# Kernel tuning notes

Measured on AMD Instinct MI355X. Metric: run time of the kernel, lower is better.

Reference implementation:

```python
import jax, jax.numpy as jnp
import numpy as np
from jax import lax

EPS = 1e-3  # BatchNorm1d eps from norm_fn
SPARSE_SHAPE = (41, 200, 176)  # (z, y, x)
IN_CH = 4


def _conv3d(x, w, stride, pad):
    # x: [N,C,D,H,W], w: [O,I,kd,kh,kw]
    return lax.conv_general_dilated(x, w, window_strides=stride, padding=pad,
                                    dimension_numbers=('NCDHW', 'OIDHW', 'NCDHW'))


def _bn_relu(y, bn, mask):
    # eval-mode BatchNorm1d over active voxels == per-channel affine; inactive sites
    # must stay exactly 0 in a sparse tensor, hence the final mask multiply.
    g, b, m, v = bn[0], bn[1], bn[2], bn[3]
    scale = g * lax.rsqrt(v + EPS)
    shift = b - m * scale
    y = y * scale[None, :, None, None, None] + shift[None, :, None, None, None]
    return jax.nn.relu(y) * mask


def _subm(x, mask, w, bn):
    # SubMConv3d: conv evaluated only at existing active sites; active set unchanged.
    kd, kh, kw = w.shape[2:]
    pad = [(kd // 2, kd // 2), (kh // 2, kh // 2), (kw // 2, kw // 2)]
    return _bn_relu(_conv3d(x, w, (1, 1, 1), pad), bn, mask)


def _spconv(x, mask, w, bn, stride, pad):
    # SparseConv3d: output active set = sites with >=1 active input in receptive field.
    pads = [(p, p) for p in pad]
    y = _conv3d(x, w, stride, pads)
    k = tuple(w.shape[2:])
    new_mask = lax.reduce_window(mask, 0.0, lax.max, (1, 1) + k, (1, 1) + tuple(stride),
                                 [(0, 0), (0, 0)] + pads)
    new_mask = (new_mask > 0).astype(x.dtype)
    return _bn_relu(y, bn, new_mask), new_mask


def setup_inputs() -> dict:
    key = jax.random.key(0)
    ks = jax.random.split(key, 16)
    D, H, W = SPARSE_SHAPE
    mask = (jax.random.uniform(ks[0], (1, 1, D, H, W)) < 0.02).astype(jnp.float32)
    x = jax.random.normal(ks[1], (1, IN_CH, D, H, W), jnp.float32) * mask
    specs = [(16, IN_CH, (3, 3, 3)), (16, 16, (3, 3, 3)),
             (32, 16, (3, 3, 3)), (32, 32, (3, 3, 3)), (32, 32, (3, 3, 3)),
             (64, 32, (3, 3, 3)), (64, 64, (3, 3, 3)), (64, 64, (3, 3, 3)),
             (64, 64, (3, 3, 3)), (64, 64, (3, 3, 3)), (64, 64, (3, 3, 3)),
             (128, 64, (3, 1, 1))]
    inp = {'x': x, 'mask': mask}
    for i, (co, ci, k) in enumerate(specs):
        kk = jax.random.fold_in(ks[2], i)
        fan = ci * k[0] * k[1] * k[2]
        inp['w%d' % i] = jax.random.normal(kk, (co, ci) + k, jnp.float32) / np.sqrt(fan).astype(np.float32)
        inp['bn%d' % i] = jnp.stack([
            jax.random.uniform(jax.random.fold_in(kk, 1), (co,), minval=0.5, maxval=1.5),
            jax.random.normal(jax.random.fold_in(kk, 2), (co,)) * 0.1,
            jax.random.normal(jax.random.fold_in(kk, 3), (co,)) * 0.1,
            jax.random.uniform(jax.random.fold_in(kk, 4), (co,), minval=0.5, maxval=1.5)])
    return inp


def reference(x, mask, w0, bn0, w1, bn1, w2, bn2, w3, bn3, w4, bn4, w5, bn5,
              w6, bn6, w7, bn7, w8, bn8, w9, bn9, w10, bn10, w11, bn11):
    h = _subm(x, mask, w0, bn0)                       # conv_input (subm1)
    h = _subm(h, mask, w1, bn1)                       # conv1 -> x_conv1
    h, m2 = _spconv(h, mask, w2, bn2, (2, 2, 2), (1, 1, 1))  # conv2 down
    h = _subm(h, m2, w3, bn3)
    h = _subm(h, m2, w4, bn4)                         # x_conv2
    h, m3 = _spconv(h, m2, w5, bn5, (2, 2, 2), (1, 1, 1))    # conv3 down
    h = _subm(h, m3, w6, bn6)
    h = _subm(h, m3, w7, bn7)                         # x_conv3
    h, m4 = _spconv(h, m3, w8, bn8, (2, 2, 2), (0, 1, 1))    # conv4 down
    h = _subm(h, m4, w9, bn9)
    h = _subm(h, m4, w10, bn10)                       # x_conv4
    out, _ = _spconv(h, m4, w11, bn11, (2, 1, 1), (0, 0, 0)) # conv_out
    N, C, Dd, Hh, Ww = out.shape                      # [1,128,2,25,22]
    return out.reshape(N, C * Dd, Hh, Ww)             # spatial_features [1,256,25,22]
```

## Files before the change

kernel.cpp:

```cpp
#include <hip/hip_runtime.h>

#define BS 256

constexpr int D1=41, H1=200, W1=176; constexpr int N1v=D1*H1*W1;
constexpr int D2=21, H2=100, W2=88;  constexpr int N2v=D2*H2*W2;
constexpr int D3=11, H3=50,  W3=44;  constexpr int N3v=D3*H3*W3;
constexpr int D4=5,  H4=25,  W4=22;  constexpr int N4v=D4*H4*W4;
constexpr int DOo=2, HOo=25, WOo=22;
constexpr int ROWS1=40960;

typedef __attribute__((ext_vector_type(8))) short bf16x8;
typedef __attribute__((ext_vector_type(4))) float f32x4;

__device__ __forceinline__ float bflo(unsigned int u){ return __uint_as_float(u<<16); }
__device__ __forceinline__ float bfhi(unsigned int u){ return __uint_as_float(u & 0xffff0000u); }
__device__ __forceinline__ unsigned short f2bf(float f){
  unsigned int x = __float_as_uint(f);
  x += 0x7fffu + ((x>>16)&1u);
  return (unsigned short)(x>>16);
}
__device__ __forceinline__ void acc8(float& acc, uint4 p, const float* __restrict__ wk, int stride){
  acc = fmaf(bflo(p.x), wk[0*stride], acc);
  acc = fmaf(bfhi(p.x), wk[1*stride], acc);
  acc = fmaf(bflo(p.y), wk[2*stride], acc);
  acc = fmaf(bfhi(p.y), wk[3*stride], acc);
  acc = fmaf(bflo(p.z), wk[4*stride], acc);
  acc = fmaf(bfhi(p.z), wk[5*stride], acc);
  acc = fmaf(bflo(p.w), wk[6*stride], acc);
  acc = fmaf(bfhi(p.w), wk[7*stride], acc);
}

struct PrepArgs {
  const float* w[12]; const float* bn[12];
  void* dst[12]; float* bias[12];
  int O[12], I[12], K[12], mode[12];
  int off[13];
};
__global__ void prep_all(PrepArgs a){
  int t = blockIdx.x*BS + threadIdx.x;
  if (t >= a.off[12]) return;
  int li = 0;
  while (t >= a.off[li+1]) li++;
  int e = t - a.off[li];
  int O=a.O[li], I=a.I[li], K=a.K[li], mode=a.mode[li];
  const float* w = a.w[li]; const float* bn = a.bn[li];
  if (mode == 2){
    int p = e/(O*32); int rem = e - p*(O*32); int o = rem>>5; int kk = rem&31;
    int tap = 2*p + (kk>=16 ? 1 : 0); int ci = kk&15;
    float g=bn[o], b=bn[O+o], m=bn[2*O+o], v=bn[3*O+o];
    float sc = g*rsqrtf(v+1e-3f);
    float val = (tap < 27) ? w[(o*I+ci)*K + tap]*sc : 0.f;
    ((unsigned short*)a.dst[li])[e] = f2bf(val);
    if (p==0 && kk==0) a.bias[li][o] = b - m*sc;
  } else if (mode == 3){
    int ci = e % I; int tmp = e / I; int dx = tmp % 3; tmp /= 3; int o = tmp % O; int g9 = tmp / O;
    float g=bn[o], b=bn[O+o], m=bn[2*O+o], v=bn[3*O+o];
    float sc = g*rsqrtf(v+1e-3f);
    int tap = g9*3 + dx;
    ((unsigned short*)a.dst[li])[e] = f2bf(w[(o*I+ci)*27 + tap]*sc);
    if (g9==0 && dx==0 && ci==0) a.bias[li][o] = b - m*sc;
  } else {
    int k = e % K; int rest = e / K; int ci = rest % I; int o = rest / I;
    float g=bn[o], b=bn[O+o], m=bn[2*O+o], v=bn[3*O+o];
    float sc = g*rsqrtf(v+1e-3f);
    ((float*)a.dst[li])[(k*I+ci)*O + o] = w[(o*I+ci)*K + k]*sc;
    if (ci==0 && k==0) a.bias[li][o] = b - m*sc;
  }
}

__global__ void build_list1_kernel(const float* __restrict__ mask,
                                   const float* __restrict__ x,
                                   unsigned short* __restrict__ xcl,
                                   int* __restrict__ I1, int* __restrict__ list1,
                                   int* __restrict__ cnt){
  constexpr int PER = 16;
  __shared__ int sc[BS]; __shared__ int sbase;
  int b = blockIdx.x, t = threadIdx.x;
  int base_s = b*BS*PER;
  unsigned int bits = 0; int c = 0;
  #pragma unroll
  for (int i=0;i<PER;i++){
    int s = base_s + i*BS + t;
    bool act = false;
    if (s < N1v){
      act = mask[s] > 0.f;
      unsigned short h0 = f2bf(x[s]),       h1 = f2bf(x[N1v+s]);
      unsigned short h2 = f2bf(x[2*N1v+s]), h3 = f2bf(x[3*N1v+s]);
      uint2 pk; pk.x = ((unsigned)h1<<16)|h0; pk.y = ((unsigned)h3<<16)|h2;
      *(uint2*)(xcl + (size_t)s*4) = pk;
    }
    bits |= (act?1u:0u) << i; c += act;
  }
  sc[t] = c;
  __syncthreads();
  for (int ofs=1; ofs<BS; ofs<<=1){
    int v = (t>=ofs) ? sc[t-ofs] : 0;
    __syncthreads();
    sc[t] += v;
    __syncthreads();
  }
  if (t == BS-1) sbase = atomicAdd(cnt, sc[t]);
  __syncthreads();
  int pos = sbase + sc[t] - c;
  #pragma unroll
  for (int i=0;i<PER;i++){
    if (bits & (1u<<i)){
      int s = base_s + i*BS + t;
      list1[pos] = s; I1[s] = pos+1; pos++;
    }
  }
}

template<int DI,int HI,int WI,int DOUT,int HOUT,int WOUT,int PZ,int PY,int PX>
__global__ void scatter_mask_kernel(const int* __restrict__ list, const int* __restrict__ cnt, int cidx,
                                    float* __restrict__ mout){
  int t = blockIdx.x*BS + threadIdx.x;
  if (t >= cnt[cidx]) return;
  int s = list[t];
  int zz = s/(HI*WI); int rem = s - zz*(HI*WI); int yy = rem/WI; int xx = rem - yy*WI;
  int az = zz + PZ, ay = yy + PY, ax = xx + PX;
  int zlo = (az-2) <= 0 ? 0 : (az-1)/2;  int zhi = min(DOUT-1, az/2);
  int ylo = (ay-2) <= 0 ? 0 : (ay-1)/2;  int yhi = min(HOUT-1, ay/2);
  int xlo = (ax-2) <= 0 ? 0 : (ax-1)/2;  int xhi = min(WOUT-1, ax/2);
  for (int zo=zlo; zo<=zhi; zo++)
    for (int yo=ylo; yo<=yhi; yo++)
      for (int xo=xlo; xo<=xhi; xo++)
        mout[(zo*HOUT+yo)*WOUT+xo] = 1.f;
}

template<int N>
__global__ void compact_mask_kernel(const float* __restrict__ mout,
                                    int* __restrict__ list, int* __restrict__ cnt1){
  __shared__ int sc[BS]; __shared__ int sbase;
  int b = blockIdx.x, t = threadIdx.x;
  int s = b*BS + t;
  bool act = (s < N) && (mout[s] > 0.f);
  int c = act ? 1 : 0;
  sc[t] = c;
  __syncthreads();
  for (int ofs=1; ofs<BS; ofs<<=1){
    int v = (t>=ofs) ? sc[t-ofs] : 0;
    __syncthreads();
    sc[t] += v;
    __syncthreads();
  }
  if (t == BS-1) sbase = atomicAdd(cnt1, sc[t]);
  __syncthreads();
  if (act) list[sbase + sc[t] - 1] = s;
}

__global__ void subm_l0_kernel(const unsigned short* __restrict__ xcl,
                               const int* __restrict__ list1, const int* __restrict__ cnt,
                               const float* __restrict__ wt, const float* __restrict__ bias,
                               unsigned short* __restrict__ fout){
  __shared__ float Wl[27*4*16];
  __shared__ float Bl[16];
  int t = threadIdx.x;
  for (int e=t; e<27*4*16; e+=BS) Wl[e] = wt[e];
  if (t < 16) Bl[t] = bias[t];
  __syncthreads();
  int row = blockIdx.x*BS + t;
  if (row >= cnt[0]) return;
  int s = list1[row];
  int z = s/(H1*W1); int r = s - z*(H1*W1); int y = r/W1; int xx = r - y*W1;
  float acc[16];
  #pragma unroll
  for (int o=0;o<16;o++) acc[o] = Bl[o];
  #pragma unroll
  for (int dz=-1; dz<=1; dz++){ int zz=z+dz; if ((unsigned)zz >= (unsigned)D1) continue;
    #pragma unroll
    for (int dy=-1; dy<=1; dy++){ int yy=y+dy; if ((unsigned)yy >= (unsigned)H1) continue;
      #pragma unroll
      for (int dx=-1; dx<=1; dx++){ int xc=xx+dx; if ((unsigned)xc >= (unsigned)W1) continue;
        int ns = (zz*H1+yy)*W1+xc;
        int k = ((dz+1)*3+(dy+1))*3+(dx+1);
        uint2 pk = *(const uint2*)(xcl + (size_t)ns*4);
        float x0 = bflo(pk.x), x1 = bfhi(pk.x), x2 = bflo(pk.y), x3 = bfhi(pk.y);
        const float* wk = Wl + k*64;
        #pragma unroll
        for (int o=0;o<16;o++)
          acc[o] = fmaf(x0, wk[o], fmaf(x1, wk[16+o], fmaf(x2, wk[32+o], fmaf(x3, wk[48+o], acc[o]))));
      }}}
  #pragma unroll
  for (int o=0;o<16;o++) fout[row*16+o] = f2bf(fmaxf(acc[o], 0.f));
}

template<int COUT,int HO,int WO,int PZ,int PY,int PX,int STR,bool DENSE_OUT>
__global__ __launch_bounds__(256)
void conv_mfma_l1_kernel(const unsigned short* __restrict__ fin,
                         const int* __restrict__ I1,
                         const int* __restrict__ list, const int* __restrict__ cnt, int cidx,
                         const unsigned short* __restrict__ wbt,
                         const float* __restrict__ bias,
                         unsigned short* __restrict__ outp){
  constexpr int BP = 40;
  constexpr int NT = COUT/16;
  __shared__ __align__(16) unsigned short B[14*COUT*BP];

  int nrows = cnt[cidx];
  int row0 = blockIdx.x*64;
  if (row0 >= nrows) return;

  int t = threadIdx.x;
  int lane = t & 63, wave = t >> 6;
  int m = lane & 15, quad = lane >> 4;

  constexpr int TOT = 14*COUT*32;
  for (int e = t*8; e < TOT; e += BS*8){
    int n = e >> 5, c = e & 31;
    *(uint4*)(&B[n*BP + c]) = *(const uint4*)(wbt + e);
  }

  int row = row0 + wave*16 + m;
  bool rv = row < nrows;
  int z=0, y=0, x=0;
  {
    int s = list[rv ? row : row0];
    z = s/(HO*WO); int rem = s - z*(HO*WO); y = rem/WO; x = rem - y*WO;
  }

  int rr[14];
  #pragma unroll
  for (int p=0;p<14;p++){
    int tap = 2*p + (quad>>1);
    rr[p] = 0;
    if (rv && tap < 27){
      int dz = tap/9, rem = tap - dz*9, dy = rem/3, dx = rem - dy*3;
      int zz = STR*z - PZ + dz, yy = STR*y - PY + dy, xx = STR*x - PX + dx;
      if ((unsigned)zz < (unsigned)D1 && (unsigned)yy < (unsigned)H1 && (unsigned)xx < (unsigned)W1)
        rr[p] = I1[(zz*H1+yy)*W1+xx];
    }
  }
  __syncthreads();

  f32x4 acc[NT];
  #pragma unroll
  for (int i=0;i<NT;i++) acc[i] = (f32x4){0.f,0.f,0.f,0.f};

  bf16x8 acur = (bf16x8){0,0,0,0,0,0,0,0};
  if (rr[0] > 0) acur = *(const bf16x8*)(fin + (size_t)(rr[0]-1)*16 + (quad&1)*8);
  #pragma unroll
  for (int p=0;p<14;p++){
    bf16x8 anext = (bf16x8){0,0,0,0,0,0,0,0};
    if (p < 13 && rr[p+1] > 0)
      anext = *(const bf16x8*)(fin + (size_t)(rr[p+1]-1)*16 + (quad&1)*8);
    #pragma unroll
    for (int nt=0; nt<NT; nt++){
      bf16x8 b = *(const bf16x8*)(&B[(p*COUT + nt*16 + m)*BP + quad*8]);
      acc[nt] = __builtin_amdgcn_mfma_f32_16x16x32_bf16(acur, b, acc[nt], 0, 0, 0);
    }
    acur = anext;
  }

  #pragma unroll
  for (int nt=0; nt<NT; nt++){
    int cout = nt*16 + m;
    float bv = bias[cout];
    #pragma unroll
    for (int rg=0; rg<4; rg++){
      int rw = row0 + wave*16 + quad*4 + rg;
      if (rw < nrows){
        float v = fmaxf(acc[nt][rg] + bv, 0.f);
        if (DENSE_OUT){
          int s = list[rw];
          outp[(size_t)s*COUT + cout] = f2bf(v);
        } else {
          outp[(size_t)rw*COUT + cout] = f2bf(v);
        }
      }
    }
  }
}

template<int CIN,int COUT,int DI,int HI,int WI,int HO,int WO,int PZ,int PY,int PX,int STR>
__global__ __launch_bounds__(256)
void conv_mfma2_kernel(const unsigned short* __restrict__ gin,
                       const int* __restrict__ list, const int* __restrict__ cnt, int cidx,
                       const unsigned short* __restrict__ wg,
                       const float* __restrict__ bias,
                       unsigned short* __restrict__ gout){
  constexpr int KW = 3*CIN;
  constexpr int BP = KW + 8;
  constexpr int NT = COUT/16;
  constexpr int KT = KW/32;
  constexpr int PREN = (COUT*KW + BS*8 - 1)/(BS*8);
  __shared__ __align__(16) unsigned short B[2][COUT*BP];

  int nrows = cnt[cidx];
  int row0 = blockIdx.x*64;
  if (row0 >= nrows) return;

  int t = threadIdx.x;
  int lane = t & 63, wave = t >> 6;
  int m = lane & 15, quad = lane >> 4;

  #pragma unroll
  for (int i=0;i<PREN;i++){
    int e = t*8 + i*BS*8;
    if (e < COUT*KW){
      int n = e / KW, c = e - n*KW;
      *(uint4*)(&B[0][n*BP + c]) = *(const uint4*)(wg + e);
    }
  }

  int row = row0 + wave*16 + m;
  bool rv = row < nrows;
  int z=0, y=0, x=0;
  {
    int s = list[rv ? row : row0];
    z = s/(HO*WO); int rem = s - z*(HO*WO); y = rem/WO; x = rem - y*WO;
  }

  auto loadA = [&](int g, bf16x8* av){
    int dz = g/3, dy = g - dz*3;
    int zz = STR*z - PZ + dz, yy = STR*y - PY + dy, xx0 = STR*x - PX;
    bool zyok = rv && (unsigned)zz < (unsigned)DI && (unsigned)yy < (unsigned)HI;
    int base = ((zz*HI + yy)*WI + xx0)*CIN;
    #pragma unroll
    for (int kt=0; kt<KT; kt++){
      int tapx = (kt*32)/CIN;
      av[kt] = (bf16x8){0,0,0,0,0,0,0,0};
      if (zyok && (unsigned)(xx0 + tapx) < (unsigned)WI)
        av[kt] = *(const bf16x8*)(gin + (size_t)(base + kt*32 + quad*8));
    }
  };

  f32x4 acc[NT];
  #pragma unroll
  for (int i=0;i<NT;i++) acc[i] = (f32x4){0.f,0.f,0.f,0.f};

  bf16x8 acur[KT], anext[KT];
  loadA(0, acur);
  __syncthreads();

  #pragma unroll
  for (int g=0; g<9; g++){
    uint4 pre[PREN];
    if (g < 8){
      const unsigned short* src = wg + (size_t)(g+1)*COUT*KW;
      #pragma unroll
      for (int i=0;i<PREN;i++){
        int e = t*8 + i*BS*8;
        pre[i] = (e < COUT*KW) ? *(const uint4*)(src + e) : (uint4){0,0,0,0};
      }
      loadA(g+1, anext);
    }
    #pragma unroll
    for (int kt=0; kt<KT; kt++){
      #pragma unroll
      for (int nt=0; nt<NT; nt++){
        bf16x8 b = *(const bf16x8*)(&B[g&1][(nt*16 + m)*BP + kt*32 + quad*8]);
        acc[nt] = __builtin_amdgcn_mfma_f32_16x16x32_bf16(acur[kt], b, acc[nt], 0, 0, 0);
      }
    }
    if (g < 8){
      #pragma unroll
      for (int i=0;i<PREN;i++){
        int e = t*8 + i*BS*8;
        if (e < COUT*KW){
          int n = e / KW, c = e - n*KW;
          *(uint4*)(&B[(g+1)&1][n*BP + c]) = pre[i];
        }
      }
      #pragma unroll
      for (int kt=0; kt<KT; kt++) acur[kt] = anext[kt];
    }
    __syncthreads();
  }

  #pragma unroll
  for (int nt=0; nt<NT; nt++){
    int cout = nt*16 + m;
    float bv = bias[cout];
    #pragma unroll
    for (int rg=0; rg<4; rg++){
      int rw = row0 + wave*16 + quad*4 + rg;
      if (rw < nrows){
        int s = list[rw];
        gout[(size_t)s*COUT + cout] = f2bf(fmaxf(acc[nt][rg] + bv, 0.f));
      }
    }
  }
}

template<int CIN,int COUT,int DI,int HI,int WI,int HO,int WO,int PZ,int PY,int PX,int STR>
__global__ __launch_bounds__(256)
void conv_tp_kernel(const unsigned short* __restrict__ gin,
                    const int* __restrict__ list, const int* __restrict__ cnt, int cidx,
                    const unsigned short* __restrict__ wg,
                    const float* __restrict__ bias,
                    unsigned short* __restrict__ gout){
  constexpr int KW = 3*CIN;
  constexpr int NT = COUT/16;
  constexpr int KT = KW/32;
  __shared__ float R[4][NT*256];

  int nrows = cnt[cidx];
  int row0 = blockIdx.x*16;
  if (row0 >= nrows) return;

  int t = threadIdx.x;
  int lane = t & 63, wave = t >> 6;
  int m = lane & 15, quad = lane >> 4;

  int row = row0 + m;
  bool rv = row < nrows;
  int z=0, y=0, x=0;
  {
    int s = list[rv ? row : row0];
    z = s/(HO*WO); int rem = s - z*(HO*WO); y = rem/WO; x = rem - y*WO;
  }

  bf16x8 av[3][KT];
  #pragma unroll
  for (int i=0;i<3;i++){
    int g = wave + i*4;
    #pragma unroll
    for (int kt=0; kt<KT; kt++) av[i][kt] = (bf16x8){0,0,0,0,0,0,0,0};
    if (g < 9){
      int dz = g/3, dy = g - dz*3;
      int zz = STR*z - PZ + dz, yy = STR*y - PY + dy, xx0 = STR*x - PX;
      bool zyok = rv && (unsigned)zz < (unsigned)DI && (unsigned)yy < (unsigned)HI;
      int base = ((zz*HI + yy)*WI + xx0)*CIN;
      #pragma unroll
      for (int kt=0; kt<KT; kt++){
        int tapx = (kt*32)/CIN;
        if (zyok && (unsigned)(xx0 + tapx) < (unsigned)WI)
          av[i][kt] = *(const bf16x8*)(gin + (size_t)(base + kt*32 + quad*8));
      }
    }
  }

  f32x4 acc[NT];
  #pragma unroll
  for (int i=0;i<NT;i++) acc[i] = (f32x4){0.f,0.f,0.f,0.f};

  #pragma unroll
  for (int i=0;i<3;i++){
    int g = wave + i*4;
    if (g < 9){
      const unsigned short* wsrc = wg + (size_t)g*COUT*KW;
      #pragma unroll
      for (int kt=0; kt<KT; kt++){
        #pragma unroll
        for (int nt=0; nt<NT; nt++){
          bf16x8 b = *(const bf16x8*)(wsrc + (size_t)(nt*16 + m)*KW + kt*32 + quad*8);
          acc[nt] = __builtin_amdgcn_mfma_f32_16x16x32_bf16(av[i][kt], b, acc[nt], 0, 0, 0);
        }
      }
    }
  }

  #pragma unroll
  for (int nt=0; nt<NT; nt++)
    #pragma unroll
    for (int rg=0; rg<4; rg++)
      R[wave][nt*256 + (quad*4+rg)*16 + m] = acc[nt][rg];
  __syncthreads();

  for (int e = t; e < 16*COUT; e += BS){
    int r = e / COUT, cout = e % COUT;
    int nt = cout >> 4, mm = cout & 15;
    int idx = nt*256 + r*16 + mm;
    float sum = R[0][idx] + R[1][idx] + R[2][idx] + R[3][idx];
    int rw = row0 + r;
    if (rw < nrows){
      int s = list[rw];
      gout[(size_t)s*COUT + cout] = f2bf(fmaxf(sum + bias[cout], 0.f));
    }
  }
}

__global__ void conv_out_kernel(const unsigned short* __restrict__ g4,
                                const float* __restrict__ m4,
                                const float* __restrict__ wt, const float* __restrict__ bias,
                                float* __restrict__ out){
  int t = blockIdx.x*BS + threadIdx.x;
  if (t >= 128*DOo*HOo*WOo) return;
  int cout = t & 127; int s = t >> 7;
  int d = s/(HOo*WOo); int r = s - d*(HOo*WOo); int h = r/WOo; int w = r - h*WOo;
  float res = 0.f;
  bool act = false;
  float acc = bias[cout];
  for (int dz=0; dz<3; dz++){
    int z4 = 2*d + dz;
    int site = (z4*H4 + h)*W4 + w;
    if (m4[site] == 0.f) continue;
    act = true;
    const uint4* fr = (const uint4*)(g4 + (size_t)site*64);
    const float* wk = wt + dz*64*128 + cout;
    #pragma unroll
    for (int q=0; q<8; q++) acc8(acc, fr[q], wk + q*8*128, 128);
  }
  if (act) res = fmaxf(acc, 0.f);
  out[((cout*DOo + d)*HOo + h)*WOo + w] = res;
}

extern "C" void kernel_launch(void* const* d_in, const int* in_sizes, int n_in,
                              void* d_out, int out_size, void* d_ws, size_t ws_size,
                              hipStream_t stream){
  const float* x    = (const float*)d_in[0];
  const float* mask = (const float*)d_in[1];
  const float* w[12]; const float* bnp[12];
  for (int i=0;i<12;i++){ w[i]=(const float*)d_in[2+2*i]; bnp[i]=(const float*)d_in[3+2*i]; }

  char* base = (char*)d_ws; size_t off = 0;
  auto alloc = [&](size_t b)->void*{ void* p = base + off; off = (off + b + 255) & ~(size_t)255; return p; };

  int* cnt   = (int*)alloc(16);
  int* I1    = (int*)alloc((size_t)N1v*4);
  unsigned short* g2a = (unsigned short*)alloc((size_t)N2v*32*2);
  unsigned short* g2b = (unsigned short*)alloc((size_t)N2v*32*2);
  unsigned short* g3a = (unsigned short*)alloc((size_t)N3v*64*2);
  unsigned short* g3b = (unsigned short*)alloc((size_t)N3v*64*2);
  unsigned short* g4a = (unsigned short*)alloc((size_t)N4v*64*2);
  unsigned short* g4b = (unsigned short*)alloc((size_t)N4v*64*2);
  float* m2 = (float*)alloc((size_t)N2v*4);
  float* m3 = (float*)alloc((size_t)N3v*4);
  float* m4 = (float*)alloc((size_t)N4v*4);
  size_t zero_bytes = off;
  unsigned short* xcl = (unsigned short*)alloc((size_t)N1v*4*2);
  int* list1 = (int*)alloc((size_t)ROWS1*4);
  unsigned short* f1a = (unsigned short*)alloc((size_t)ROWS1*16*2);
  unsigned short* f1b = (unsigned short*)alloc((size_t)ROWS1*16*2);
  int* list2 = (int*)alloc((size_t)N2v*4);
  int* list3 = (int*)alloc((size_t)N3v*4);
  int* list4 = (int*)alloc((size_t)N4v*4);

  static const int Oa[12]={16,16,32,32,32,64,64,64,64,64,64,128};
  static const int Ia[12]={ 4,16,16,32,32,32,64,64,64,64,64, 64};
  static const int Ka[12]={27,27,27,27,27,27,27,27,27,27,27,  3};
  static const int Ma[12]={ 0, 2, 2, 3, 3, 3, 3, 3, 3, 3, 3,  0};
  float* wt[12]; float* bs[12]; unsigned short* wbt[12];
  for (int i=0;i<12;i++){
    bs[i] = (float*)alloc((size_t)Oa[i]*4);
    wt[i]=nullptr; wbt[i]=nullptr;
    if (Ma[i]==0)      wt[i]  = (float*)alloc((size_t)Oa[i]*Ia[i]*Ka[i]*4);
    else if (Ma[i]==3) wbt[i] = (unsigned short*)alloc((size_t)Oa[i]*Ia[i]*27*2);
    else               wbt[i] = (unsigned short*)alloc((size_t)14*Oa[i]*32*2);
  }

  hipMemsetAsync(base, 0, zero_bytes, stream);

  PrepArgs pa;
  pa.off[0] = 0;
  for (int i=0;i<12;i++){
    pa.w[i]=w[i]; pa.bn[i]=bnp[i]; pa.bias[i]=bs[i];
    pa.O[i]=Oa[i]; pa.I[i]=Ia[i]; pa.K[i]=Ka[i]; pa.mode[i]=Ma[i];
    pa.dst[i] = (Ma[i]==0) ? (void*)wt[i] : (void*)wbt[i];
    int tot = (Ma[i]==2) ? 14*Oa[i]*32 : Oa[i]*Ia[i]*Ka[i];
    pa.off[i+1] = pa.off[i] + tot;
  }
  prep_all<<<(pa.off[12]+BS-1)/BS, BS, 0, stream>>>(pa);

  build_list1_kernel<<<(N1v + BS*16 - 1)/(BS*16), BS, 0, stream>>>(mask, x, xcl, I1, list1, cnt);

  subm_l0_kernel<<<(ROWS1+BS-1)/BS, BS, 0, stream>>>(xcl, list1, cnt, wt[0], bs[0], f1a);
  conv_mfma_l1_kernel<16,H1,W1,1,1,1,1,false><<<ROWS1/64, 256, 0, stream>>>
      (f1a, I1, list1, cnt, 0, wbt[1], bs[1], f1b);

  scatter_mask_kernel<D1,H1,W1,D2,H2,W2,1,1,1><<<(ROWS1+BS-1)/BS, BS, 0, stream>>>(list1, cnt, 0, m2);
  compact_mask_kernel<N2v><<<(N2v+BS-1)/BS, BS, 0, stream>>>(m2, list2, cnt+1);
  conv_mfma_l1_kernel<32,H2,W2,1,1,1,2,true><<<(N2v+63)/64, 256, 0, stream>>>
      (f1b, I1, list2, cnt, 1, wbt[2], bs[2], g2a);

  {
    int nb = (N2v + 63)/64;
    conv_mfma2_kernel<32,32,D2,H2,W2,H2,W2,1,1,1,1><<<nb, 256, 0, stream>>>(g2a, list2, cnt, 1, wbt[3], bs[3], g2b);
    conv_mfma2_kernel<32,32,D2,H2,W2,H2,W2,1,1,1,1><<<nb, 256, 0, stream>>>(g2b, list2, cnt, 1, wbt[4], bs[4], g2a);
  }

  scatter_mask_kernel<D2,H2,W2,D3,H3,W3,1,1,1><<<(N2v+BS-1)/BS, BS, 0, stream>>>(list2, cnt, 1, m3);
  compact_mask_kernel<N3v><<<(N3v+BS-1)/BS, BS, 0, stream>>>(m3, list3, cnt+2);
  {
    conv_tp_kernel<32,64,D2,H2,W2,H3,W3,1,1,1,2><<<(N3v+15)/16, 256, 0, stream>>>(g2a, list3, cnt, 2, wbt[5], bs[5], g3a);
    int nb = (N3v + 63)/64;
    conv_mfma2_kernel<64,64,D3,H3,W3,H3,W3,1,1,1,1><<<nb, 256, 0, stream>>>(g3a, list3, cnt, 2, wbt[6], bs[6], g3b);
    conv_mfma2_kernel<64,64,D3,H3,W3,H3,W3,1,1,1,1><<<nb, 256, 0, stream>>>(g3b, list3, cnt, 2, wbt[7], bs[7], g3a);
  }

  scatter_mask_kernel<D3,H3,W3,D4,H4,W4,0,1,1><<<(N3v+BS-1)/BS, BS, 0, stream>>>(list3, cnt, 2, m4);
  compact_mask_kernel<N4v><<<(N4v+BS-1)/BS, BS, 0, stream>>>(m4, list4, cnt+3);
  {
    int nb = (N4v + 15)/16;
    conv_tp_kernel<64,64,D3,H3,W3,H4,W4,0,1,1,2><<<nb, 256, 0, stream>>>(g3a, list4, cnt, 3, wbt[8], bs[8], g4a);
    conv_tp_kernel<64,64,D4,H4,W4,H4,W4,1,1,1,1><<<nb, 256, 0, stream>>>(g4a, list4, cnt, 3, wbt[9], bs[9], g4b);
    conv_tp_kernel<64,64,D4,H4,W4,H4,W4,1,1,1,1><<<nb, 256, 0, stream>>>(g4b, list4, cnt, 3, wbt[10], bs[10], g4a);
  }

  conv_out_kernel<<<(128*DOo*HOo*WOo)/BS, BS, 0, stream>>>(g4a, m4, wt[11], bs[11], (float*)d_out);
}
```

Baseline: 360.9 us.

## Preload all gathered activations and add single-stage 32-channel subm conv kernel

In the L1 conv kernel, all 14 activation gathers are now issued up front, before the barrier, instead of being software-pipelined one step ahead. This gives more memory-level parallelism at the cost of more registers. A new specialized kernel for the 32->32 layer-2 submanifold convs loads all 9 weight groups into shared memory once, without double buffering. It also preloads all 27 activation fragments into registers before running the MFMA loop. The larger shared memory and register footprint may lower occupancy.

```diff
diff --git a/kernel.cpp b/kernel.cpp
--- a/kernel.cpp
+++ b/kernel.cpp
@@ -231,25 +231,25 @@
         rr[p] = I1[(zz*H1+yy)*W1+xx];
     }
   }
+  bf16x8 av[14];
+  #pragma unroll
+  for (int p=0;p<14;p++){
+    av[p] = (bf16x8){0,0,0,0,0,0,0,0};
+    if (rr[p] > 0) av[p] = *(const bf16x8*)(fin + (size_t)(rr[p]-1)*16 + (quad&1)*8);
+  }
   __syncthreads();
 
   f32x4 acc[NT];
   #pragma unroll
   for (int i=0;i<NT;i++) acc[i] = (f32x4){0.f,0.f,0.f,0.f};
 
-  bf16x8 acur = (bf16x8){0,0,0,0,0,0,0,0};
-  if (rr[0] > 0) acur = *(const bf16x8*)(fin + (size_t)(rr[0]-1)*16 + (quad&1)*8);
   #pragma unroll
   for (int p=0;p<14;p++){
-    bf16x8 anext = (bf16x8){0,0,0,0,0,0,0,0};
-    if (p < 13 && rr[p+1] > 0)
-      anext = *(const bf16x8*)(fin + (size_t)(rr[p+1]-1)*16 + (quad&1)*8);
     #pragma unroll
     for (int nt=0; nt<NT; nt++){
       bf16x8 b = *(const bf16x8*)(&B[(p*COUT + nt*16 + m)*BP + quad*8]);
-      acc[nt] = __builtin_amdgcn_mfma_f32_16x16x32_bf16(acur, b, acc[nt], 0, 0, 0);
-    }
-    acur = anext;
+      acc[nt] = __builtin_amdgcn_mfma_f32_16x16x32_bf16(av[p], b, acc[nt], 0, 0, 0);
+    }
   }
 
   #pragma unroll
@@ -267,6 +267,84 @@
         } else {
           outp[(size_t)rw*COUT + cout] = f2bf(v);
         }
+      }
+    }
+  }
+}
+
+template<int DI,int HI,int WI,int PZ,int PY,int PX>
+__global__ __launch_bounds__(256)
+void conv_mfma2s_kernel(const unsigned short* __restrict__ gin,
+                        const int* __restrict__ list, const int* __restrict__ cnt, int cidx,
+                        const unsigned short* __restrict__ wg,
+                        const float* __restrict__ bias,
+                        unsigned short* __restrict__ gout){
+  constexpr int CIN=32, COUT=32, KW=96, BP=104, NT=2, KT=3;
+  __shared__ __align__(16) unsigned short B[9*COUT*BP];
+
+  int nrows = cnt[cidx];
+  int row0 = blockIdx.x*64;
+  if (row0 >= nrows) return;
+
+  int t = threadIdx.x;
+  int lane = t & 63, wave = t >> 6;
+  int m = lane & 15, quad = lane >> 4;
+
+  for (int e = t*8; e < 9*COUT*KW; e += BS*8){
+    int n = e / KW, c = e - n*KW;
+    *(uint4*)(&B[n*BP + c]) = *(const uint4*)(wg + e);
+  }
+
+  int row = row0 + wave*16 + m;
+  bool rv = row < nrows;
+  int z=0, y=0, x=0;
+  {
+    int s = list[rv ? row : row0];
+    z = s/(HI*WI); int rem = s - z*(HI*WI); y = rem/WI; x = rem - y*WI;
+  }
+
+  bf16x8 av[9][KT];
+  #pragma unroll
+  for (int g=0; g<9; g++){
+    int dz = g/3, dy = g - dz*3;
+    int zz = z - PZ + dz, yy = y - PY + dy, xx0 = x - PX;
+    bool zyok = rv && (unsigned)zz < (unsigned)DI && (unsigned)yy < (unsigned)HI;
+    int base = ((zz*HI + yy)*WI + xx0)*CIN;
+    #pragma unroll
+    for (int kt=0; kt<KT; kt++){
+      av[g][kt] = (bf16x8){0,0,0,0,0,0,0,0};
+      if (zyok && (unsigned)(xx0 + kt) < (unsigned)WI)
+        av[g][kt] = *(const bf16x8*)(gin + (size_t)(base + kt*32 + quad*8));
+    }
+  }
+  __syncthreads();
+
+  f32x4 acc[NT];
+  #pragma unroll
+  for (int i=0;i<NT;i++) acc[i] = (f32x4){0.f,0.f,0.f,0.f};
+
+  #pragma unroll
+  for (int g=0; g<9; g++){
+    #pragma unroll
+    for (int kt=0; kt<KT; kt++){
+      #pragma unroll
+      for (int nt=0; nt<NT; nt++){
+        bf16x8 b = *(const bf16x8*)(&B[(g*COUT + nt*16 + m)*BP + kt*32 + quad*8]);
+        acc[nt] = __builtin_amdgcn_mfma_f32_16x16x32_bf16(av[g][kt], b, acc[nt], 0, 0, 0);
+      }
+    }
+  }
+
+  #pragma unroll
+  for (int nt=0; nt<NT; nt++){
+    int cout = nt*16 + m;
+    float bv = bias[cout];
+    #pragma unroll
+    for (int rg=0; rg<4; rg++){
+      int rw = row0 + wave*16 + quad*4 + rg;
+      if (rw < nrows){
+        int s = list[rw];
+        gout[(size_t)s*COUT + cout] = f2bf(fmaxf(acc[nt][rg] + bv, 0.f));
       }
     }
   }
@@ -566,8 +644,8 @@
 
   {
     int nb = (N2v + 63)/64;
-    conv_mfma2_kernel<32,32,D2,H2,W2,H2,W2,1,1,1,1><<<nb, 256, 0, stream>>>(g2a, list2, cnt, 1, wbt[3], bs[3], g2b);
-    conv_mfma2_kernel<32,32,D2,H2,W2,H2,W2,1,1,1,1><<<nb, 256, 0, stream>>>(g2b, list2, cnt, 1, wbt[4], bs[4], g2a);
+    conv_mfma2s_kernel<D2,H2,W2,1,1,1><<<nb, 256, 0, stream>>>(g2a, list2, cnt, 1, wbt[3], bs[3], g2b);
+    conv_mfma2s_kernel<D2,H2,W2,1,1,1><<<nb, 256, 0, stream>>>(g2b, list2, cnt, 1, wbt[4], bs[4], g2a);
   }
 
   scatter_mask_kernel<D2,H2,W2,D3,H3,W3,1,1,1><<<(N2v+BS-1)/BS, BS, 0, stream>>>(list2, cnt, 1, m3);
```

After: 378.8 us. +5.0%, slower.
